# Kernel optimization log

Measured on AMD Instinct MI355X. Metric: run time of the kernel, lower is better.

## Reference

```python
import jax, jax.numpy as jnp
import numpy as np

N_QUBITS = 10
DIM = 2 ** N_QUBITS
N_POINTS = 64
D_FEAT = 10
N_LAYERS = 5

# bit tables: bits[:, q] = q-th least-significant bit of the state index.
# kron order in the original builds angles[n-1] x ... x angles[0], so angle q acts on bit q.
_bits = ((np.arange(DIM)[:, None] >> np.arange(N_QUBITS)[None, :]) & 1).astype(np.float32)
BITS_C = jnp.asarray(_bits - 0.5)  # (DIM, n): b_q - 1/2 -> rz diag phase coeffs
# crz ring: crz_matrix(i+1,...) is diagonal phase exp(i*theta*b_{i}*(b_{i+1}-1/2)) (control i, target i+1);
# close_ring is control n-1, target 0.
_ctrl = np.concatenate([np.arange(N_QUBITS - 1), [N_QUBITS - 1]])
_tgt = np.concatenate([np.arange(1, N_QUBITS), [0]])
RING_COEF = jnp.asarray(_bits[:, _ctrl] * (_bits[:, _tgt] - 0.5))  # (DIM, n)
H_GATES = jnp.broadcast_to(
    jnp.asarray((np.array([[1, 1], [1, -1]]) / np.sqrt(2)).astype(np.complex64)),
    (N_QUBITS, 2, 2))


def rz_diag(x, start):
    # rz_layer kron order: qubit q gets angle x[(start + n-1-q) % d]; rz = diag(e^{-it/2}, e^{it/2})
    idx = (start + N_QUBITS - 1 - np.arange(N_QUBITS)) % D_FEAT
    return jnp.exp(1j * (BITS_C @ x[idx]))  # (DIM,) complex64


def ring_diag(angles):
    return jnp.exp(1j * (RING_COEF @ angles))  # (DIM,) complex64


def ry_gates(angles):
    c, s = jnp.cos(0.5 * angles), jnp.sin(0.5 * angles)
    # (n, 2, 2): [[c, -s], [s, c]]
    return jnp.stack([jnp.stack([c, -s], -1), jnp.stack([s, c], -1)], -2).astype(jnp.complex64)


def apply_1q(state, gates):
    # apply gates[q] (2x2) to qubit q (axis n-1-q of the (2,)*n reshaped state)
    psi = state.reshape((2,) * N_QUBITS)
    for q in range(N_QUBITS):
        ax = N_QUBITS - 1 - q
        psi = jnp.moveaxis(jnp.tensordot(gates[q], psi, axes=([1], [ax])), 0, ax)
    return psi.reshape(DIM)


def block_f(state, x, bp, start):
    state = apply_1q(state, H_GATES)
    state = state * rz_diag(x, start)
    state = apply_1q(state, ry_gates(bp[0]))
    return state * ring_diag(bp[1])


def adj_block_f(state, x, bp, start):
    state = state * jnp.conj(ring_diag(bp[1]))
    state = apply_1q(state, ry_gates(-bp[0]))  # ry(t)^dagger = ry(-t)
    state = state * jnp.conj(rz_diag(x, start))
    return apply_1q(state, H_GATES)  # H is self-adjoint


def pair_prob(x1, x2, params):
    state = jnp.zeros((DIM,), jnp.complex64).at[0].set(1.0)
    for j in range(N_LAYERS):
        state = block_f(state, x1, params[j], j * N_QUBITS)
    for k in range(N_LAYERS):
        # faithful to original: start = (num_q - k - 1) * num_q (uses num_q, not n_layers)
        state = adj_block_f(state, x2, params[N_LAYERS - 1 - k], (N_QUBITS - k - 1) * N_QUBITS)
    a = state[0]
    return jnp.real(a) ** 2 + jnp.imag(a) ** 2  # |<0|U2^dag U1|0>|^2


def _kta(data, labels, params):
    x1 = jnp.repeat(data, N_POINTS, axis=0)   # point i of each pair
    x2 = jnp.tile(data, (N_POINTS, 1))        # point j of each pair
    k = jax.vmap(pair_prob, in_axes=(0, 0, None))(x1, x2, params)  # (N*N,)
    lm = (labels[:, None] * labels[None, :]).reshape(-1)
    kp = jnp.sum(lm * k)
    return kp / jnp.sqrt(jnp.sum(k * k) * jnp.sum(lm * lm))


def setup_inputs() -> dict:
    key = jax.random.key(0)
    k1, k2, k3 = jax.random.split(key, 3)
    data = jax.random.normal(k1, (N_POINTS, D_FEAT), jnp.float32)
    labels = jnp.where(jax.random.normal(k2, (N_POINTS,)) >= 0, 1.0, -1.0).astype(jnp.float32)
    params = jax.random.uniform(k3, (N_LAYERS, 2, N_QUBITS), jnp.float32, 0.0, 2.0 * np.pi)
    return {"data": data, "labels": labels, "params": params}


def reference(data, labels, params):
    return _kta(data, labels, params)
```

## Files before the change

kernel.cpp:

```cpp
#include <hip/hip_runtime.h>
#include <math.h>

#define NQ 10
#define DIM 1024
#define NPTS 64
#define DFEAT 10
#define NLAYERS 5
#define REGS 16

__global__ __launch_bounds__(64) void state_kernel(
    const float* __restrict__ data,
    const float* __restrict__ params,
    float2* __restrict__ psi)
{
    const int i    = blockIdx.x;
    const int lane = threadIdx.x;

    float xr[NQ];
#pragma unroll
    for (int q = 0; q < NQ; ++q) xr[q] = data[i * DFEAT + (9 - q)];

    float rzs[REGS], rzc[REGS];
    {
        float lanep = 0.f;
#pragma unroll
        for (int q = 0; q < 6; ++q)
            lanep += (((lane >> q) & 1) ? 0.5f : -0.5f) * xr[q];
#pragma unroll
        for (int r = 0; r < REGS; ++r) {
            float ph = lanep;
#pragma unroll
            for (int q = 6; q < NQ; ++q)
                ph += (((r >> (q - 6)) & 1) ? 0.5f : -0.5f) * xr[q];
            rzs[r] = __sinf(ph);
            rzc[r] = __cosf(ph);
        }
    }

    float re[REGS], im[REGS];
#pragma unroll
    for (int r = 0; r < REGS; ++r) { re[r] = 0.f; im[r] = 0.f; }
    if (lane == 0) re[0] = 1.f;

    const float is2 = 0.70710678118654752440f;

    for (int layer = 0; layer < NLAYERS; ++layer) {
        const float* ry = params + layer * 2 * NQ;
        const float* rg = params + layer * 2 * NQ + NQ;

        for (int q = 0; q < 6; ++q) {
            const int mask = 1 << q;
            float pr[REGS], pi[REGS];
#pragma unroll
            for (int r = 0; r < REGS; ++r) {
                pr[r] = __shfl_xor(re[r], mask, 64);
                pi[r] = __shfl_xor(im[r], mask, 64);
            }
            const bool hi = (lane & mask) != 0;
#pragma unroll
            for (int r = 0; r < REGS; ++r) {
                re[r] = hi ? (pr[r] - re[r]) * is2 : (re[r] + pr[r]) * is2;
                im[r] = hi ? (pi[r] - im[r]) * is2 : (im[r] + pi[r]) * is2;
            }
        }
#pragma unroll
        for (int q = 6; q < NQ; ++q) {
            const int m = 1 << (q - 6);
#pragma unroll
            for (int r = 0; r < REGS; ++r) {
                if (!(r & m)) {
                    const int r1 = r | m;
                    float a0r = re[r], a0i = im[r], a1r = re[r1], a1i = im[r1];
                    re[r]  = (a0r + a1r) * is2;  im[r]  = (a0i + a1i) * is2;
                    re[r1] = (a0r - a1r) * is2;  im[r1] = (a0i - a1i) * is2;
                }
            }
        }

#pragma unroll
        for (int r = 0; r < REGS; ++r) {
            float s = rzs[r], c = rzc[r];
            float nr = re[r] * c - im[r] * s;
            float ni = re[r] * s + im[r] * c;
            re[r] = nr; im[r] = ni;
        }

        for (int q = 0; q < 6; ++q) {
            const int mask = 1 << q;
            const float h = 0.5f * ry[q];
            const float s = __sinf(h), c = __cosf(h);
            float pr[REGS], pi[REGS];
#pragma unroll
            for (int r = 0; r < REGS; ++r) {
                pr[r] = __shfl_xor(re[r], mask, 64);
                pi[r] = __shfl_xor(im[r], mask, 64);
            }
            const bool hi = (lane & mask) != 0;
#pragma unroll
            for (int r = 0; r < REGS; ++r) {
                re[r] = hi ? s * pr[r] + c * re[r] : c * re[r] - s * pr[r];
                im[r] = hi ? s * pi[r] + c * im[r] : c * im[r] - s * pi[r];
            }
        }
#pragma unroll
        for (int q = 6; q < NQ; ++q) {
            const int m = 1 << (q - 6);
            const float h = 0.5f * ry[q];
            const float s = __sinf(h), c = __cosf(h);
#pragma unroll
            for (int r = 0; r < REGS; ++r) {
                if (!(r & m)) {
                    const int r1 = r | m;
                    float a0r = re[r], a0i = im[r], a1r = re[r1], a1i = im[r1];
                    re[r]  = c * a0r - s * a1r;  im[r]  = c * a0i - s * a1i;
                    re[r1] = s * a0r + c * a1r;  im[r1] = s * a0i + c * a1i;
                }
            }
        }

#pragma unroll
        for (int r = 0; r < REGS; ++r) {
            const int idx = (r << 6) | lane;
            float ph = 0.f;
#pragma unroll
            for (int n = 0; n < NQ; ++n) {
                const int bc = (idx >> n) & 1;
                const int bt = (idx >> ((n + 1) % NQ)) & 1;
                float t = bc ? (bt ? 0.5f : -0.5f) : 0.f;
                ph += t * rg[n];
            }
            float s = __sinf(ph), c = __cosf(ph);
            float nr = re[r] * c - im[r] * s;
            float ni = re[r] * s + im[r] * c;
            re[r] = nr; im[r] = ni;
        }
    }

    float2* out = psi + i * DIM;
#pragma unroll
    for (int r = 0; r < REGS; ++r)
        out[(r << 6) | lane] = make_float2(re[r], im[r]);
}

__global__ __launch_bounds__(256) void gram_kernel(
    const float4* __restrict__ psi4,
    float* __restrict__ Kbuf)
{
    const int wave = threadIdx.x >> 6;
    const int lane = threadIdx.x & 63;
    const int p    = blockIdx.x * 4 + wave;
    const int i    = p >> 6;
    const int j    = p & 63;
    if (j < i) return;

    const float4* a = psi4 + i * (DIM / 2);
    const float4* b = psi4 + j * (DIM / 2);

    float zr = 0.f, zi = 0.f;
#pragma unroll
    for (int r = 0; r < 8; ++r) {
        const int k = (r << 6) | lane;
        float4 av = a[k], bv = b[k];
        zr += bv.x * av.x + bv.y * av.y + bv.z * av.z + bv.w * av.w;
        zi += bv.x * av.y - bv.y * av.x + bv.z * av.w - bv.w * av.z;
    }
#pragma unroll
    for (int off = 32; off; off >>= 1) {
        zr += __shfl_xor(zr, off, 64);
        zi += __shfl_xor(zi, off, 64);
    }
    if (lane == 0) {
        const float k = zr * zr + zi * zi;
        Kbuf[p] = k;
        Kbuf[(j << 6) | i] = k;
    }
}

__global__ __launch_bounds__(256) void reduce_kernel(
    const float* __restrict__ Kbuf,
    const float* __restrict__ labels,
    float* __restrict__ out)
{
    __shared__ float sm[3][4];
    const int tid  = threadIdx.x;
    const int lane = tid & 63;
    const int wave = tid >> 6;

    float slk = 0.f, skk = 0.f, sll = 0.f;
#pragma unroll
    for (int it = 0; it < (NPTS * NPTS) / 256; ++it) {
        const int p = it * 256 + tid;
        const float K  = Kbuf[p];
        const float lm = labels[p >> 6] * labels[p & 63];
        slk += lm * K;
        skk += K * K;
        sll += lm * lm;
    }
#pragma unroll
    for (int off = 32; off; off >>= 1) {
        slk += __shfl_xor(slk, off, 64);
        skk += __shfl_xor(skk, off, 64);
        sll += __shfl_xor(sll, off, 64);
    }
    if (lane == 0) { sm[0][wave] = slk; sm[1][wave] = skk; sm[2][wave] = sll; }
    __syncthreads();
    if (tid == 0) {
        float a = sm[0][0] + sm[0][1] + sm[0][2] + sm[0][3];
        float b = sm[1][0] + sm[1][1] + sm[1][2] + sm[1][3];
        float c = sm[2][0] + sm[2][1] + sm[2][2] + sm[2][3];
        out[0] = a / sqrtf(b * c);
    }
}

extern "C" void kernel_launch(void* const* d_in, const int* in_sizes, int n_in,
                              void* d_out, int out_size, void* d_ws, size_t ws_size,
                              hipStream_t stream) {
    const float* data   = (const float*)d_in[0];
    const float* labels = (const float*)d_in[1];
    const float* params = (const float*)d_in[2];
    float* out = (float*)d_out;

    float2* psi  = (float2*)d_ws;
    float*  Kbuf = (float*)((char*)d_ws + (size_t)NPTS * DIM * sizeof(float2));

    state_kernel <<<NPTS,             64, 0, stream>>>(data, params, psi);
    gram_kernel  <<<NPTS * NPTS / 4, 256, 0, stream>>>((const float4*)psi, Kbuf);
    reduce_kernel<<<1,               256, 0, stream>>>(Kbuf, labels, out);
}
```

Baseline: 91.20 us.

## Fuse H·RZ·RY into one 2x2 gate per qubit and drop unitaries that cancel

Result: slower. 111.6 us (+22.3%).

```diff
diff --git a/kernel.cpp b/kernel.cpp
--- a/kernel.cpp
+++ b/kernel.cpp
@@ -7,6 +7,8 @@
 #define DFEAT 10
 #define NLAYERS 5
 #define REGS 16
+
+#define IS2 0.70710678118654752440f
 
 __global__ __launch_bounds__(64) void state_kernel(
     const float* __restrict__ data,
@@ -16,124 +18,141 @@
     const int i    = blockIdx.x;
     const int lane = threadIdx.x;
 
-    float xr[NQ];
-#pragma unroll
-    for (int q = 0; q < NQ; ++q) xr[q] = data[i * DFEAT + (9 - q)];
-
-    float rzs[REGS], rzc[REGS];
+    float cxq[NQ], sxq[NQ];
+#pragma unroll
+    for (int q = 0; q < NQ; ++q) {
+        float h = 0.5f * data[i * DFEAT + (9 - q)];
+        cxq[q] = __cosf(h);
+        sxq[q] = __sinf(h);
+    }
+
+    float re[REGS], im[REGS];
+
     {
-        float lanep = 0.f;
-#pragma unroll
-        for (int q = 0; q < 6; ++q)
-            lanep += (((lane >> q) & 1) ? 0.5f : -0.5f) * xr[q];
+        const float* ry = params;
+        float u0r[NQ], u0i[NQ], u1r[NQ], u1i[NQ];
+#pragma unroll
+        for (int q = 0; q < NQ; ++q) {
+            float h = 0.5f * ry[q];
+            float c = __cosf(h), s = __sinf(h);
+            float p = (c + s) * IS2, qm = (c - s) * IS2;
+            u0r[q] =  qm * cxq[q];  u0i[q] = -p  * sxq[q];
+            u1r[q] =  p  * cxq[q];  u1i[q] =  qm * sxq[q];
+        }
+        float Lr = ((lane >> 0) & 1) ? u1r[0] : u0r[0];
+        float Li = ((lane >> 0) & 1) ? u1i[0] : u0i[0];
+#pragma unroll
+        for (int q = 1; q < 6; ++q) {
+            float fr = ((lane >> q) & 1) ? u1r[q] : u0r[q];
+            float fi = ((lane >> q) & 1) ? u1i[q] : u0i[q];
+            float nr = Lr * fr - Li * fi;
+            float ni = Lr * fi + Li * fr;
+            Lr = nr; Li = ni;
+        }
 #pragma unroll
         for (int r = 0; r < REGS; ++r) {
-            float ph = lanep;
-#pragma unroll
-            for (int q = 6; q < NQ; ++q)
-                ph += (((r >> (q - 6)) & 1) ? 0.5f : -0.5f) * xr[q];
-            rzs[r] = __sinf(ph);
-            rzc[r] = __cosf(ph);
-        }
-    }
-
-    float re[REGS], im[REGS];
-#pragma unroll
-    for (int r = 0; r < REGS; ++r) { re[r] = 0.f; im[r] = 0.f; }
-    if (lane == 0) re[0] = 1.f;
-
-    const float is2 = 0.70710678118654752440f;
-
-    for (int layer = 0; layer < NLAYERS; ++layer) {
-        const float* ry = params + layer * 2 * NQ;
-        const float* rg = params + layer * 2 * NQ + NQ;
-
+            float Rr = (r & 1) ? u1r[6] : u0r[6];
+            float Ri = (r & 1) ? u1i[6] : u0i[6];
+#pragma unroll
+            for (int q = 7; q < NQ; ++q) {
+                const int b = (r >> (q - 6)) & 1;
+                float fr = b ? u1r[q] : u0r[q];
+                float fi = b ? u1i[q] : u0i[q];
+                float nr = Rr * fr - Ri * fi;
+                float ni = Rr * fi + Ri * fr;
+                Rr = nr; Ri = ni;
+            }
+            re[r] = Lr * Rr - Li * Ri;
+            im[r] = Lr * Ri + Li * Rr;
+        }
+    }
+
+#define RING_DIAG(LAYER)                                                      \
+    {                                                                         \
+        const float* rg = params + (LAYER) * 2 * NQ + NQ;                     \
+        float lanep = 0.f;                                                    \
+        _Pragma("unroll")                                                     \
+        for (int n = 0; n < 5; ++n) {                                         \
+            float t = (((lane >> (n + 1)) & 1) ? 0.5f : -0.5f) * rg[n];       \
+            lanep += ((lane >> n) & 1) ? t : 0.f;                             \
+        }                                                                     \
+        const float t5 = ((lane >> 5) & 1) ? rg[5] : 0.f;                     \
+        const float t9 = ((lane & 1) ? 0.5f : -0.5f) * rg[9];                 \
+        _Pragma("unroll")                                                     \
+        for (int r = 0; r < REGS; ++r) {                                      \
+            float ph = lanep + ((r & 1) ? 0.5f : -0.5f) * t5;                 \
+            if (r & 8) ph += t9;                                              \
+            if (r & 1) ph += ((r & 2) ? 0.5f : -0.5f) * rg[6];                \
+            if (r & 2) ph += ((r & 4) ? 0.5f : -0.5f) * rg[7];                \
+            if (r & 4) ph += ((r & 8) ? 0.5f : -0.5f) * rg[8];                \
+            float s = __sinf(ph), c = __cosf(ph);                             \
+            float nr = re[r] * c - im[r] * s;                                 \
+            float ni = re[r] * s + im[r] * c;                                 \
+            re[r] = nr; im[r] = ni;                                           \
+        }                                                                     \
+    }
+
+    RING_DIAG(0)
+
+#pragma unroll
+    for (int L = 1; L < NLAYERS; ++L) {
+        const float* ry = params + L * 2 * NQ;
+        float mp[NQ], mq[NQ];
+#pragma unroll
+        for (int q = 0; q < NQ; ++q) {
+            float c, s;
+            if (L == NLAYERS - 1) { c = 1.f; s = 0.f; }
+            else { float h = 0.5f * ry[q]; c = __cosf(h); s = __sinf(h); }
+            mp[q] = (c + s) * IS2;
+            mq[q] = (c - s) * IS2;
+        }
+
+#pragma unroll
         for (int q = 0; q < 6; ++q) {
-            const int mask = 1 << q;
+            const float m00r =  mq[q] * cxq[q], m00i = -mp[q] * sxq[q];
+            const float m01r =  mp[q] * cxq[q], m01i = -mq[q] * sxq[q];
+            const float m10r =  m01r,           m10i =  mq[q] * sxq[q];
+            const float m11r = -m00r,           m11i =  m00i;
+            const int bit = (lane >> q) & 1;
+            const float msr = bit ? m11r : m00r, msi = bit ? m11i : m00i;
+            const float mpr = bit ? m10r : m01r, mpi = bit ? m10i : m01i;
             float pr[REGS], pi[REGS];
 #pragma unroll
             for (int r = 0; r < REGS; ++r) {
-                pr[r] = __shfl_xor(re[r], mask, 64);
-                pi[r] = __shfl_xor(im[r], mask, 64);
-            }
-            const bool hi = (lane & mask) != 0;
+                pr[r] = __shfl_xor(re[r], 1 << q, 64);
+                pi[r] = __shfl_xor(im[r], 1 << q, 64);
+            }
 #pragma unroll
             for (int r = 0; r < REGS; ++r) {
-                re[r] = hi ? (pr[r] - re[r]) * is2 : (re[r] + pr[r]) * is2;
-                im[r] = hi ? (pi[r] - im[r]) * is2 : (im[r] + pi[r]) * is2;
-            }
-        }
+                float nr = msr * re[r] - msi * im[r] + mpr * pr[r] - mpi * pi[r];
+                float ni = msr * im[r] + msi * re[r] + mpr * pi[r] + mpi * pr[r];
+                re[r] = nr; im[r] = ni;
+            }
+        }
+
 #pragma unroll
         for (int q = 6; q < NQ; ++q) {
             const int m = 1 << (q - 6);
+            const float m00r =  mq[q] * cxq[q], m00i = -mp[q] * sxq[q];
+            const float m01r =  mp[q] * cxq[q], m01i = -mq[q] * sxq[q];
+            const float m10r =  m01r,           m10i =  mq[q] * sxq[q];
+            const float m11r = -m00r,           m11i =  m00i;
 #pragma unroll
             for (int r = 0; r < REGS; ++r) {
                 if (!(r & m)) {
                     const int r1 = r | m;
                     float a0r = re[r], a0i = im[r], a1r = re[r1], a1i = im[r1];
-                    re[r]  = (a0r + a1r) * is2;  im[r]  = (a0i + a1i) * is2;
-                    re[r1] = (a0r - a1r) * is2;  im[r1] = (a0i - a1i) * is2;
+                    re[r]  = m00r * a0r - m00i * a0i + m01r * a1r - m01i * a1i;
+                    im[r]  = m00r * a0i + m00i * a0r + m01r * a1i + m01i * a1r;
+                    re[r1] = m10r * a0r - m10i * a0i + m11r * a1r - m11i * a1i;
+                    im[r1] = m10r * a0i + m10i * a0r + m11r * a1i + m11i * a1r;
                 }
             }
         }
 
-#pragma unroll
-        for (int r = 0; r < REGS; ++r) {
-            float s = rzs[r], c = rzc[r];
-            float nr = re[r] * c - im[r] * s;
-            float ni = re[r] * s + im[r] * c;
-            re[r] = nr; im[r] = ni;
-        }
-
-        for (int q = 0; q < 6; ++q) {
-            const int mask = 1 << q;
-            const float h = 0.5f * ry[q];
-            const float s = __sinf(h), c = __cosf(h);
-            float pr[REGS], pi[REGS];
-#pragma unroll
-            for (int r = 0; r < REGS; ++r) {
-                pr[r] = __shfl_xor(re[r], mask, 64);
-                pi[r] = __shfl_xor(im[r], mask, 64);
-            }
-            const bool hi = (lane & mask) != 0;
-#pragma unroll
-            for (int r = 0; r < REGS; ++r) {
-                re[r] = hi ? s * pr[r] + c * re[r] : c * re[r] - s * pr[r];
-                im[r] = hi ? s * pi[r] + c * im[r] : c * im[r] - s * pi[r];
-            }
-        }
-#pragma unroll
-        for (int q = 6; q < NQ; ++q) {
-            const int m = 1 << (q - 6);
-            const float h = 0.5f * ry[q];
-            const float s = __sinf(h), c = __cosf(h);
-#pragma unroll
-            for (int r = 0; r < REGS; ++r) {
-                if (!(r & m)) {
-                    const int r1 = r | m;
-                    float a0r = re[r], a0i = im[r], a1r = re[r1], a1i = im[r1];
-                    re[r]  = c * a0r - s * a1r;  im[r]  = c * a0i - s * a1i;
-                    re[r1] = s * a0r + c * a1r;  im[r1] = s * a0i + c * a1i;
-                }
-            }
-        }
-
-#pragma unroll
-        for (int r = 0; r < REGS; ++r) {
-            const int idx = (r << 6) | lane;
-            float ph = 0.f;
-#pragma unroll
-            for (int n = 0; n < NQ; ++n) {
-                const int bc = (idx >> n) & 1;
-                const int bt = (idx >> ((n + 1) % NQ)) & 1;
-                float t = bc ? (bt ? 0.5f : -0.5f) : 0.f;
-                ph += t * rg[n];
-            }
-            float s = __sinf(ph), c = __cosf(ph);
-            float nr = re[r] * c - im[r] * s;
-            float ni = re[r] * s + im[r] * c;
-            re[r] = nr; im[r] = ni;
-        }
+        if (L == 1) RING_DIAG(1)
+        if (L == 2) RING_DIAG(2)
+        if (L == 3) RING_DIAG(3)
     }
 
     float2* out = psi + i * DIM;
```
